# Kernel tuning notes

Measured on AMD Instinct MI355X. Metric: run time of the kernel, lower is better.

The kernel has to match this reference:

```python
import jax, jax.numpy as jnp
import numpy as np

KH, KW = 3, 3
KN = KH * KW  # kernel_n = 9


def _grid_offset(H, W):
    # Faithful to TF build(): stack(meshgrid(ij)).reshape(-1, 2) -- note this
    # interleaves i- and j- grids in an unusual layout; we replicate it exactly.
    init = jnp.stack(jnp.meshgrid(jnp.arange(KH), jnp.arange(KW), indexing='ij'))
    init = init.reshape(-1, 2).astype(jnp.float32)  # (KN, 2)
    ph, pw = (KH - 1) // 2, (KW - 1) // 2
    g = jnp.stack(
        jnp.meshgrid(jnp.arange(-ph, H - ph), jnp.arange(-pw, W - pw), indexing='ij'),
        axis=-1,
    ).astype(jnp.float32)  # (H, W, 2)
    return g[:, :, None, :] + init[None, None]  # (H, W, KN, 2)


def _bilinear_sample(x, coords):
    # x: (B, H, W, C); coords: (B, H, W, KN, 2) with (row, col) float coords.
    B = x.shape[0]
    y, xc = coords[..., 0], coords[..., 1]
    y0 = jnp.floor(y).astype(jnp.int32)
    y1 = jnp.ceil(y).astype(jnp.int32)   # ceil (not floor+1), faithful to TF code
    x0 = jnp.floor(xc).astype(jnp.int32)
    x1 = jnp.ceil(xc).astype(jnp.int32)
    bidx = jnp.arange(B)[:, None, None, None]

    def g(yy, xx):
        return x[bidx, yy, xx]  # (B, H, W, KN, C)

    v_lt = g(y0, x0)
    v_rb = g(y1, x1)
    v_lb = g(y0, x1)  # (lt_row, rb_col) per TF coords_lb
    v_rt = g(y1, x0)  # (rb_row, lt_col) per TF coords_rt
    fy = (y - y0.astype(y.dtype))[..., None]
    fx = (xc - x0.astype(xc.dtype))[..., None]
    v_t = v_lt + (v_rt - v_lt) * fy
    v_b = v_lb + (v_rb - v_lb) * fy
    return v_t + (v_b - v_t) * fx  # (B, H, W, KN, C)


def setup_inputs() -> dict:
    key = jax.random.key(0)
    k1, k2, k3 = jax.random.split(key, 3)
    B, H, W, C, F = 8, 64, 64, 128, 128
    x = jax.random.normal(k1, (B, H, W, C), dtype=jnp.float32)
    offset = jax.random.normal(k2, (B, H, W, 2 * KN), dtype=jnp.float32)
    Wk = jax.random.truncated_normal(k3, -2.0, 2.0, (KN, C, F), dtype=jnp.float32) * 0.02
    b = jnp.zeros((F,), dtype=jnp.float32)
    return {"x": x, "offset": offset, "W": Wk, "b": b}


def reference(x, offset, W, b):
    B, H, Wd, C = x.shape
    coords = _grid_offset(H, Wd)[None] + offset.reshape(B, H, Wd, KN, 2)
    coords = jnp.stack(
        [
            jnp.clip(coords[..., 0], 0.0, float(H - 1)),
            jnp.clip(coords[..., 1], 0.0, float(Wd - 1)),
        ],
        axis=-1,
    )
    deform = _bilinear_sample(x, coords)  # (B, H, W, KN, C)
    # conv3d with (1,1,KN,C,F) filter, VALID == contraction over (KN, C)
    out = jnp.einsum('bhwnc,ncf->bhwf', deform, W) + b
    return out
```

## Files before the change

### kernel.cpp

```cpp
#include <hip/hip_runtime.h>
#include <stdint.h>

#define KN 9
#define HH 64
#define WW 64
#define CC 128
#define FF 128
#define TM 64
#define NT 512
#define LDK 136

typedef __bf16 bf16x8 __attribute__((ext_vector_type(8)));
typedef float f32x4 __attribute__((ext_vector_type(4)));
typedef unsigned short us8 __attribute__((ext_vector_type(8)));

__constant__ float c_init_i[KN] = {0.f,0.f,1.f,2.f,2.f,1.f,0.f,2.f,1.f};
__constant__ float c_init_j[KN] = {0.f,1.f,1.f,2.f,0.f,2.f,1.f,0.f,2.f};

static __device__ inline float bf2f(unsigned short u) {
    union { unsigned u; float f; } v; v.u = ((unsigned)u) << 16; return v.f;
}

__global__ void prep_kernel(const float* __restrict__ Wk, unsigned short* __restrict__ Wt,
                            const float* __restrict__ x, unsigned short* __restrict__ xb) {
    __shared__ unsigned short t[32][33];
    const int tid = threadIdx.x;
    if (blockIdx.x >= 144) {
        int i = ((blockIdx.x - 144) * 256 + tid) * 8;
        float4 a = *(const float4*)(x + i);
        float4 b = *(const float4*)(x + i + 4);
        us8 o;
        o[0] = __builtin_bit_cast(unsigned short, (__bf16)a.x);
        o[1] = __builtin_bit_cast(unsigned short, (__bf16)a.y);
        o[2] = __builtin_bit_cast(unsigned short, (__bf16)a.z);
        o[3] = __builtin_bit_cast(unsigned short, (__bf16)a.w);
        o[4] = __builtin_bit_cast(unsigned short, (__bf16)b.x);
        o[5] = __builtin_bit_cast(unsigned short, (__bf16)b.y);
        o[6] = __builtin_bit_cast(unsigned short, (__bf16)b.z);
        o[7] = __builtin_bit_cast(unsigned short, (__bf16)b.w);
        *(us8*)(xb + i) = o;
        return;
    }
    const int n  = blockIdx.x >> 4;
    const int tf = blockIdx.x & 3;
    const int tc = (blockIdx.x >> 2) & 3;
    const int g  = tid >> 5;
    const int l  = tid & 31;
#pragma unroll
    for (int r = 0; r < 4; ++r) {
        int cl = g * 4 + r;
        t[cl][l] = __builtin_bit_cast(unsigned short,
                    (__bf16)Wk[(n << 14) + ((tc * 32 + cl) << 7) + (tf * 32 + l)]);
    }
    __syncthreads();
#pragma unroll
    for (int r = 0; r < 4; ++r) {
        int o   = r * 256 + tid;
        int b   = o >> 9;
        int q   = (o >> 7) & 3;
        int col = (o >> 3) & 15;
        int e   = o & 7;
        Wt[(((n * 4 + tc) * 4 + tf) << 10) + o] = t[q * 8 + e][b * 16 + col];
    }
}

#define ISSUE(n_, s_, S) do {                                          \
    int p_ = (s_) >> 4; int ch_ = ((s_) & 15) * 8;                     \
    int lt_o = cB[p_][n_][0], rb_o = cB[p_][n_][1];                    \
    int rt_o = (rb_o & 0x7E000) | (lt_o & 0x1F80);                     \
    int lb_o = (lt_o & 0x7E000) | (rb_o & 0x1F80);                     \
    lt##S = *(const us8*)(bb16 + lt_o + ch_);                          \
    rt##S = *(const us8*)(bb16 + rt_o + ch_);                          \
    lb##S = *(const us8*)(bb16 + lb_o + ch_);                          \
    rb##S = *(const us8*)(bb16 + rb_o + ch_);                          \
    __builtin_amdgcn_sched_barrier(0);                                 \
  } while (0)

#define CONSUME(n_, s_, S) do {                                        \
    int p_ = (s_) >> 4; int ch_ = ((s_) & 15) * 8;                     \
    float fy_ = cF[p_][n_][0], fx_ = cF[p_][n_][1];                    \
    us8 pk_;                                                           \
    _Pragma("unroll")                                                  \
    for (int j = 0; j < 8; ++j) {                                      \
      float v0_ = bf2f(lt##S[j]), v1_ = bf2f(rt##S[j]);                \
      float v2_ = bf2f(lb##S[j]), v3_ = bf2f(rb##S[j]);                \
      float vt_ = v0_ + (v1_ - v0_) * fy_;                             \
      float vb_ = v2_ + (v3_ - v2_) * fy_;                             \
      float r_  = vt_ + (vb_ - vt_) * fx_;                             \
      pk_[j] = __builtin_bit_cast(unsigned short, (__bf16)r_);         \
    }                                                                  \
    *(us8*)&As[d][p_][ch_] = pk_;                                      \
  } while (0)

#define LOADB(n_) do {                                                 \
    const unsigned short* wn_ = wbase + ((n_) << 14);                  \
    bfr0 = *(const us8*)(wn_);                                         \
    bfr1 = *(const us8*)(wn_ + 512);                                   \
    bfr2 = *(const us8*)(wn_ + 4096);                                  \
    bfr3 = *(const us8*)(wn_ + 4096 + 512);                            \
    bfr4 = *(const us8*)(wn_ + 8192);                                  \
    bfr5 = *(const us8*)(wn_ + 8192 + 512);                            \
    bfr6 = *(const us8*)(wn_ + 12288);                                 \
    bfr7 = *(const us8*)(wn_ + 12288 + 512);                           \
    __builtin_amdgcn_sched_barrier(0);                                 \
  } while (0)

#define MSTEP(ks_, B0, B1) do {                                        \
    bf16x8 a0_ = __builtin_bit_cast(bf16x8, *(const us8*)(&As[d][mtile + col][(ks_) * 32 + quad * 8]));      \
    bf16x8 a1_ = __builtin_bit_cast(bf16x8, *(const us8*)(&As[d][mtile + 16 + col][(ks_) * 32 + quad * 8])); \
    acc00 = __builtin_amdgcn_mfma_f32_16x16x32_bf16(a0_, __builtin_bit_cast(bf16x8, B0), acc00, 0, 0, 0);    \
    acc01 = __builtin_amdgcn_mfma_f32_16x16x32_bf16(a0_, __builtin_bit_cast(bf16x8, B1), acc01, 0, 0, 0);    \
    acc10 = __builtin_amdgcn_mfma_f32_16x16x32_bf16(a1_, __builtin_bit_cast(bf16x8, B0), acc10, 0, 0, 0);    \
    acc11 = __builtin_amdgcn_mfma_f32_16x16x32_bf16(a1_, __builtin_bit_cast(bf16x8, B1), acc11, 0, 0, 0);    \
  } while (0)

__launch_bounds__(NT, 4)
__global__ void deform_kernel(const unsigned short* __restrict__ xb,
                              const float* __restrict__ off,
                              const unsigned short* __restrict__ Wt,
                              const float* __restrict__ bias,
                              float* __restrict__ out) {
    __shared__ unsigned short As[2][TM][LDK];
    __shared__ int   cB[TM][KN][2];
    __shared__ float cF[TM][KN][2];

    const int tid = threadIdx.x;
    const int bb   = blockIdx.x & 7;
    const int hh   = blockIdx.x >> 3;
    const int pix0 = (bb << 12) + (hh << 6);

    for (int t = tid; t < TM * KN; t += NT) {
        int p = t & (TM - 1);
        int n = t >> 6;
        float2 o = *(const float2*)(off + (size_t)(pix0 + p) * (2 * KN) + 2 * n);
        float y = (float)(hh - 1) + c_init_i[n] + o.x;
        float x = (float)(p - 1) + c_init_j[n] + o.y;
        y = fminf(fmaxf(y, 0.f), 63.f);
        x = fminf(fmaxf(x, 0.f), 63.f);
        float y0f = floorf(y), x0f = floorf(x);
        int y0 = (int)y0f, x0 = (int)x0f;
        int y1 = (int)ceilf(y), x1 = (int)ceilf(x);
        cB[p][n][0] = (y0 << 13) | (x0 << 7);
        cB[p][n][1] = (y1 << 13) | (x1 << 7);
        cF[p][n][0] = y - y0f;
        cF[p][n][1] = x - x0f;
    }

    const int wave = tid >> 6;
    const int lane = tid & 63;
    const int quad = lane >> 4;
    const int col  = lane & 15;
    const int mtile = (wave & 1) * 32;
    const int ntile = (wave >> 1) * 32;
    const int gi    = wave >> 1;

    f32x4 acc00 = {0.f,0.f,0.f,0.f}, acc01 = {0.f,0.f,0.f,0.f};
    f32x4 acc10 = {0.f,0.f,0.f,0.f}, acc11 = {0.f,0.f,0.f,0.f};

    const unsigned short* bb16  = xb + ((size_t)bb << 19);
    const unsigned short* wbase = Wt + (gi << 10) + (lane << 3);

    us8 ltA, rtA, lbA, rbA;
    us8 ltB, rtB, lbB, rbB;
    us8 bfr0, bfr1, bfr2, bfr3, bfr4, bfr5, bfr6, bfr7;

    __syncthreads();

    ISSUE(0, tid, A);
    int d = 0;

    for (int n = 0; n < KN; ++n, d ^= 1) {
        ISSUE(n, tid + NT, B);
        LOADB(n);
        CONSUME(n, tid, A);
        ISSUE(n + 1 < KN ? n + 1 : n, tid, A);
        CONSUME(n, tid + NT, B);

        asm volatile("s_waitcnt lgkmcnt(0)" ::: "memory");
        __builtin_amdgcn_s_barrier();

        MSTEP(0, bfr0, bfr1);
        MSTEP(1, bfr2, bfr3);
        MSTEP(2, bfr4, bfr5);
        MSTEP(3, bfr6, bfr7);
    }

#pragma unroll
    for (int b = 0; b < 2; ++b) {
        int f = ntile + b * 16 + col;
        float bv = bias[f];
        const f32x4 ac0 = b ? acc01 : acc00;
        const f32x4 ac1 = b ? acc11 : acc10;
#pragma unroll
        for (int r = 0; r < 4; ++r) {
            int pr0 = pix0 + mtile + quad * 4 + r;
            out[(size_t)pr0 * FF + f] = ac0[r] + bv;
            int pr1 = pr0 + 16;
            out[(size_t)pr1 * FF + f] = ac1[r] + bv;
        }
    }
}

extern "C" void kernel_launch(void* const* d_in, const int* in_sizes, int n_in,
                              void* d_out, int out_size, void* d_ws, size_t ws_size,
                              hipStream_t stream) {
    const float* x    = (const float*)d_in[0];
    const float* off  = (const float*)d_in[1];
    const float* Wk   = (const float*)d_in[2];
    const float* bias = (const float*)d_in[3];
    float* out = (float*)d_out;
    unsigned short* Wt = (unsigned short*)d_ws;
    unsigned short* xb = (unsigned short*)d_ws + 147456;

    prep_kernel<<<144 + 2048, 256, 0, stream>>>(Wk, Wt, x, xb);
    deform_kernel<<<(8 * HH * WW) / TM, NT, 0, stream>>>(xb, off, Wt, bias, out);
}
```

Measured before the change: 100.5 us.

## Halve pixel tile to 32, software-pipeline tap loop with double-buffered LDS

Shrinks each block's tile from 64 to 32 pixels, doubling the grid to 1024 blocks. Each wave now computes a 32x16 output slice instead of 32x32, so it holds fewer accumulators and weight registers, and the launch bound rises to 6 blocks per SM. The tap loop is restructured so each thread gathers one pixel-channel group per tap. It alternates between two LDS buffers, issuing the next tap's gathers and weight loads while the current tap's MFMAs run. The cost is that each block reloads the full weight tensor for half as many pixels, doubling weight traffic.

```diff
diff --git a/kernel.cpp b/kernel.cpp
--- a/kernel.cpp
+++ b/kernel.cpp
@@ -2,11 +2,9 @@
 #include <stdint.h>
 
 #define KN 9
-#define HH 64
-#define WW 64
 #define CC 128
 #define FF 128
-#define TM 64
+#define TM 32
 #define NT 512
 #define LDK 136
 
@@ -64,21 +62,19 @@
     }
 }
 
-#define ISSUE(n_, s_, S) do {                                          \
-    int p_ = (s_) >> 4; int ch_ = ((s_) & 15) * 8;                     \
-    int lt_o = cB[p_][n_][0], rb_o = cB[p_][n_][1];                    \
+#define ISSUE(n_, S) do {                                              \
+    int lt_o = cB[ip][n_][0], rb_o = cB[ip][n_][1];                    \
     int rt_o = (rb_o & 0x7E000) | (lt_o & 0x1F80);                     \
     int lb_o = (lt_o & 0x7E000) | (rb_o & 0x1F80);                     \
-    lt##S = *(const us8*)(bb16 + lt_o + ch_);                          \
-    rt##S = *(const us8*)(bb16 + rt_o + ch_);                          \
-    lb##S = *(const us8*)(bb16 + lb_o + ch_);                          \
-    rb##S = *(const us8*)(bb16 + rb_o + ch_);                          \
+    lt##S = *(const us8*)(bb16 + lt_o + icg);                          \
+    rt##S = *(const us8*)(bb16 + rt_o + icg);                          \
+    lb##S = *(const us8*)(bb16 + lb_o + icg);                          \
+    rb##S = *(const us8*)(bb16 + rb_o + icg);                          \
     __builtin_amdgcn_sched_barrier(0);                                 \
   } while (0)
 
-#define CONSUME(n_, s_, S) do {                                        \
-    int p_ = (s_) >> 4; int ch_ = ((s_) & 15) * 8;                     \
-    float fy_ = cF[p_][n_][0], fx_ = cF[p_][n_][1];                    \
+#define CONSUME(n_, S, d_) do {                                        \
+    float fy_ = cF[ip][n_][0], fx_ = cF[ip][n_][1];                    \
     us8 pk_;                                                           \
     _Pragma("unroll")                                                  \
     for (int j = 0; j < 8; ++j) {                                      \
@@ -89,32 +85,35 @@
       float r_  = vt_ + (vb_ - vt_) * fx_;                             \
       pk_[j] = __builtin_bit_cast(unsigned short, (__bf16)r_);         \
     }                                                                  \
-    *(us8*)&As[d][p_][ch_] = pk_;                                      \
+    *(us8*)&As[d_][ip][icg] = pk_;                                     \
   } while (0)
 
 #define LOADB(n_) do {                                                 \
-    const unsigned short* wn_ = wbase + ((n_) << 14);                  \
-    bfr0 = *(const us8*)(wn_);                                         \
-    bfr1 = *(const us8*)(wn_ + 512);                                   \
-    bfr2 = *(const us8*)(wn_ + 4096);                                  \
-    bfr3 = *(const us8*)(wn_ + 4096 + 512);                            \
-    bfr4 = *(const us8*)(wn_ + 8192);                                  \
-    bfr5 = *(const us8*)(wn_ + 8192 + 512);                            \
-    bfr6 = *(const us8*)(wn_ + 12288);                                 \
-    bfr7 = *(const us8*)(wn_ + 12288 + 512);                           \
+    bfr0 = *(const us8*)(wbase + ((n_) << 14));                        \
+    bfr1 = *(const us8*)(wbase + ((n_) << 14) + 4096);                 \
+    bfr2 = *(const us8*)(wbase + ((n_) << 14) + 8192);                 \
+    bfr3 = *(const us8*)(wbase + ((n_) << 14) + 12288);                \
     __builtin_amdgcn_sched_barrier(0);                                 \
   } while (0)
 
-#define MSTEP(ks_, B0, B1) do {                                        \
-    bf16x8 a0_ = __builtin_bit_cast(bf16x8, *(const us8*)(&As[d][mtile + col][(ks_) * 32 + quad * 8]));      \
-    bf16x8 a1_ = __builtin_bit_cast(bf16x8, *(const us8*)(&As[d][mtile + 16 + col][(ks_) * 32 + quad * 8])); \
-    acc00 = __builtin_amdgcn_mfma_f32_16x16x32_bf16(a0_, __builtin_bit_cast(bf16x8, B0), acc00, 0, 0, 0);    \
-    acc01 = __builtin_amdgcn_mfma_f32_16x16x32_bf16(a0_, __builtin_bit_cast(bf16x8, B1), acc01, 0, 0, 0);    \
-    acc10 = __builtin_amdgcn_mfma_f32_16x16x32_bf16(a1_, __builtin_bit_cast(bf16x8, B0), acc10, 0, 0, 0);    \
-    acc11 = __builtin_amdgcn_mfma_f32_16x16x32_bf16(a1_, __builtin_bit_cast(bf16x8, B1), acc11, 0, 0, 0);    \
-  } while (0)
-
-__launch_bounds__(NT, 4)
+#define MSTEP(d_, ks_, B_) do {                                        \
+    bf16x8 a0_ = __builtin_bit_cast(bf16x8, *(const us8*)(&As[d_][col][(ks_) * 32 + quad * 8]));      \
+    bf16x8 a1_ = __builtin_bit_cast(bf16x8, *(const us8*)(&As[d_][16 + col][(ks_) * 32 + quad * 8])); \
+    acc0 = __builtin_amdgcn_mfma_f32_16x16x32_bf16(a0_, __builtin_bit_cast(bf16x8, B_), acc0, 0, 0, 0); \
+    acc1 = __builtin_amdgcn_mfma_f32_16x16x32_bf16(a1_, __builtin_bit_cast(bf16x8, B_), acc1, 0, 0, 0); \
+  } while (0)
+
+#define MTAP(d_) do {                                                  \
+    MSTEP(d_, 0, bfr0); MSTEP(d_, 1, bfr1);                            \
+    MSTEP(d_, 2, bfr2); MSTEP(d_, 3, bfr3);                            \
+  } while (0)
+
+#define BAR() do {                                                     \
+    asm volatile("s_waitcnt lgkmcnt(0)" ::: "memory");                 \
+    __builtin_amdgcn_s_barrier();                                      \
+  } while (0)
+
+__launch_bounds__(NT, 6)
 __global__ void deform_kernel(const unsigned short* __restrict__ xb,
                               const float* __restrict__ off,
                               const unsigned short* __restrict__ Wt,
@@ -126,15 +125,16 @@
 
     const int tid = threadIdx.x;
     const int bb   = blockIdx.x & 7;
-    const int hh   = blockIdx.x >> 3;
-    const int pix0 = (bb << 12) + (hh << 6);
+    const int rr   = blockIdx.x >> 3;
+    const int pix0 = (bb << 12) + (rr << 5);
 
     for (int t = tid; t < TM * KN; t += NT) {
         int p = t & (TM - 1);
-        int n = t >> 6;
+        int n = t >> 5;
+        int pg = (rr << 5) + p;
         float2 o = *(const float2*)(off + (size_t)(pix0 + p) * (2 * KN) + 2 * n);
-        float y = (float)(hh - 1) + c_init_i[n] + o.x;
-        float x = (float)(p - 1) + c_init_j[n] + o.y;
+        float y = (float)((pg >> 6) - 1) + c_init_i[n] + o.x;
+        float x = (float)((pg & 63) - 1) + c_init_j[n] + o.y;
         y = fminf(fmaxf(y, 0.f), 63.f);
         x = fminf(fmaxf(x, 0.f), 63.f);
         float y0f = floorf(y), x0f = floorf(x);
@@ -150,53 +150,49 @@
     const int lane = tid & 63;
     const int quad = lane >> 4;
     const int col  = lane & 15;
-    const int mtile = (wave & 1) * 32;
-    const int ntile = (wave >> 1) * 32;
-    const int gi    = wave >> 1;
-
-    f32x4 acc00 = {0.f,0.f,0.f,0.f}, acc01 = {0.f,0.f,0.f,0.f};
-    f32x4 acc10 = {0.f,0.f,0.f,0.f}, acc11 = {0.f,0.f,0.f,0.f};
+
+    f32x4 acc0 = {0.f,0.f,0.f,0.f}, acc1 = {0.f,0.f,0.f,0.f};
 
     const unsigned short* bb16  = xb + ((size_t)bb << 19);
-    const unsigned short* wbase = Wt + (gi << 10) + (lane << 3);
+    const unsigned short* wbase = Wt + (wave << 9) + (lane << 3);
+
+    const int ip  = tid >> 4;
+    const int icg = (tid & 15) * 8;
 
     us8 ltA, rtA, lbA, rbA;
     us8 ltB, rtB, lbB, rbB;
-    us8 bfr0, bfr1, bfr2, bfr3, bfr4, bfr5, bfr6, bfr7;
+    us8 bfr0, bfr1, bfr2, bfr3;
 
     __syncthreads();
 
-    ISSUE(0, tid, A);
-    int d = 0;
-
-    for (int n = 0; n < KN; ++n, d ^= 1) {
-        ISSUE(n, tid + NT, B);
-        LOADB(n);
-        CONSUME(n, tid, A);
-        ISSUE(n + 1 < KN ? n + 1 : n, tid, A);
-        CONSUME(n, tid + NT, B);
-
-        asm volatile("s_waitcnt lgkmcnt(0)" ::: "memory");
-        __builtin_amdgcn_s_barrier();
-
-        MSTEP(0, bfr0, bfr1);
-        MSTEP(1, bfr2, bfr3);
-        MSTEP(2, bfr4, bfr5);
-        MSTEP(3, bfr6, bfr7);
-    }
-
-#pragma unroll
-    for (int b = 0; b < 2; ++b) {
-        int f = ntile + b * 16 + col;
-        float bv = bias[f];
-        const f32x4 ac0 = b ? acc01 : acc00;
-        const f32x4 ac1 = b ? acc11 : acc10;
-#pragma unroll
-        for (int r = 0; r < 4; ++r) {
-            int pr0 = pix0 + mtile + quad * 4 + r;
-            out[(size_t)pr0 * FF + f] = ac0[r] + bv;
-            int pr1 = pr0 + 16;
-            out[(size_t)pr1 * FF + f] = ac1[r] + bv;
+    ISSUE(0, A);
+    LOADB(0);
+
+    for (int n = 0; n < 8; n += 2) {
+        ISSUE(n + 1, B);
+        CONSUME(n, A, 0);
+        BAR();
+        MTAP(0);
+        LOADB(n + 1);
+        ISSUE(n + 2, A);
+        CONSUME(n + 1, B, 1);
+        BAR();
+        MTAP(1);
+        LOADB(n + 2);
+    }
+    CONSUME(8, A, 0);
+    BAR();
+    MTAP(0);
+
+    const int fcol = (wave << 4) + col;
+    const float bv = bias[fcol];
+#pragma unroll
+    for (int r = 0; r < 2; ++r) {
+        const f32x4 ac = r ? acc1 : acc0;
+#pragma unroll
+        for (int g = 0; g < 4; ++g) {
+            int pr = pix0 + (r << 4) + (quad << 2) + g;
+            out[(size_t)pr * FF + fcol] = ac[g] + bv;
         }
     }
 }
@@ -213,5 +209,5 @@
     unsigned short* xb = (unsigned short*)d_ws + 147456;
 
     prep_kernel<<<144 + 2048, 256, 0, stream>>>(Wk, Wt, x, xb);
-    deform_kernel<<<(8 * HH * WW) / TM, NT, 0, stream>>>(xb, off, Wt, bias, out);
-}
+    deform_kernel<<<(8 * 64 * 64) / TM, NT, 0, stream>>>(xb, off, Wt, bias, out);
+}
```

Result: slower. 141.6 us (+40.9%).
